# Optimization experiments

Hardware: AMD Instinct MI355X
Metric: run time of the kernel (lower is better)

## Reference

```python
import jax, jax.numpy as jnp
import numpy as np

NEG_MASK = -999999.0  # additive mask constant from the original module


def setup_inputs() -> dict:
    key = jax.random.key(0)
    k1, k2, k3, k4 = jax.random.split(key, 4)
    B, P, H, D = 64, 512, 512, 512
    premise_batch = jax.random.normal(k1, (B, P, D), dtype=jnp.float32)
    hypothesis_batch = jax.random.normal(k2, (B, H, D), dtype=jnp.float32)
    premise_mask = jax.random.randint(k3, (B, P), 0, 2, dtype=jnp.int32)
    hypothesis_mask = jax.random.randint(k4, (B, H), 0, 2, dtype=jnp.int32)
    return {
        "premise_batch": premise_batch,
        "premise_mask": premise_mask,
        "hypothesis_batch": hypothesis_batch,
        "hypothesis_mask": hypothesis_mask,
    }


def reference(premise_batch, premise_mask, hypothesis_batch, hypothesis_mask):
    # similarity: [B, P, H]
    sim = jnp.einsum("bpd,bhd->bph", premise_batch, hypothesis_batch)
    # additive -999999 masks, exactly as in the torch source
    hyp_pad = (hypothesis_mask == 0).astype(sim.dtype)[:, None, :]   # [B,1,H]
    pre_pad = (premise_mask == 0).astype(sim.dtype)[:, :, None]      # [B,P,1]
    sim_hyp = sim + NEG_MASK * hyp_pad
    sim_pre = sim + NEG_MASK * pre_pad
    attention_a = jax.nn.softmax(sim_pre, axis=2)  # softmax over hypothesis dim
    attention_b = jax.nn.softmax(sim_hyp, axis=1)  # softmax over premise dim
    attended_premises = jnp.einsum("bph,bhd->bpd", attention_a, hypothesis_batch)
    attended_hypothesis = jnp.einsum("bph,bpd->bhd", attention_b, premise_batch)
    return (attended_premises, attended_hypothesis)
```

## Files before the change

### kernel.cpp

```cpp
#include <hip/hip_runtime.h>
#include <hip/hip_bf16.h>
#include <math.h>

#define NEG_MASK -999999.0f

constexpr int BB = 64, PP = 512, HH = 512, DD = 512;

typedef _Float16 h8    __attribute__((ext_vector_type(8)));
typedef float    f32x4 __attribute__((ext_vector_type(4)));
typedef float    f32x2 __attribute__((ext_vector_type(2)));

#define MFMA16(a, b, c) __builtin_amdgcn_mfma_f32_16x16x32_f16(a, b, c, 0, 0, 0)

__device__ __forceinline__ int swz(int row, int kb) {
  return (row * 64 + kb) ^ ((row & 7) << 4);
}

__device__ __forceinline__ void gload16(const void* g, void* l) {
  __builtin_amdgcn_global_load_lds(
      (const __attribute__((address_space(1))) unsigned int*)g,
      (__attribute__((address_space(3))) unsigned int*)l, 16, 0, 0);
}

__device__ __forceinline__ void inv_swz(int x, int& row, int& kb) {
  row = ((x >> 7) << 1) | (((x >> 6) & 1) ^ ((x >> 8) & 1));
  kb = (x & 63) ^ ((row & 3) << 4);
}

__global__ __launch_bounds__(256) void tcvt(const float* __restrict__ src,
                                            _Float16* __restrict__ dst) {
  const int b = blockIdx.z;
  const int d0 = blockIdx.x * 64, n0 = blockIdx.y * 64;
  src += (size_t)b * 512 * 512;
  dst += (size_t)b * 512 * 512;
  const int dl = threadIdx.x & 63, nch = (threadIdx.x >> 6) * 16;
  const float* ps = src + (size_t)(n0 + nch) * 512 + d0 + dl;
  h8 o[2];
#pragma unroll
  for (int e = 0; e < 16; ++e)
    o[e >> 3][e & 7] = (_Float16)ps[(size_t)e * 512];
  _Float16* pd = dst + (size_t)(d0 + dl) * 512 + n0 + nch;
  *reinterpret_cast<h8*>(pd) = o[0];
  *reinterpret_cast<h8*>(pd + 8) = o[1];
}

__global__ __launch_bounds__(256, 2) void sim_mfma(const float* __restrict__ pre,
                                                   const float* __restrict__ hyp,
                                                   float* __restrict__ sim) {
  const int b = blockIdx.z;
  const int p0 = blockIdx.y * 128, h0 = blockIdx.x * 128;

  __shared__ __align__(16) char sAh[8192], sAl[8192], sBh[8192], sBl[8192];

  const int t = threadIdx.x;
  const int r = t >> 1, kh = t & 1;
  const int lane = t & 63, wid = t >> 6;
  const int l15 = lane & 15, l4 = lane >> 4;
  const int wr = (wid >> 1) * 64, wc = (wid & 1) * 64;

  f32x4 acc[4][4] = {};

  const float* pA = pre + (size_t)b * PP * DD + (size_t)(p0 + r) * DD + kh * 16;
  const float* pB = hyp + (size_t)b * HH * DD + (size_t)(h0 + r) * DD + kh * 16;

  for (int kk = 0; kk < DD; kk += 32) {
    f32x4 ra[4], rb[4];
#pragma unroll
    for (int c = 0; c < 4; ++c) {
      ra[c] = *reinterpret_cast<const f32x4*>(pA + kk + c * 4);
      rb[c] = *reinterpret_cast<const f32x4*>(pB + kk + c * 4);
    }
    __syncthreads();
    h8 vah[2], val[2], vbh[2], vbl[2];
#pragma unroll
    for (int c = 0; c < 4; ++c)
#pragma unroll
      for (int e = 0; e < 4; ++e) {
        const int idx = c * 4 + e;
        float fa = ra[c][e], fb = rb[c][e];
        _Float16 ha = (_Float16)fa, hb = (_Float16)fb;
        vah[idx >> 3][idx & 7] = ha;
        val[idx >> 3][idx & 7] = (_Float16)(fa - (float)ha);
        vbh[idx >> 3][idx & 7] = hb;
        vbl[idx >> 3][idx & 7] = (_Float16)(fb - (float)hb);
      }
    *reinterpret_cast<h8*>(sAh + swz(r, kh * 32)) = vah[0];
    *reinterpret_cast<h8*>(sAh + swz(r, kh * 32 + 16)) = vah[1];
    *reinterpret_cast<h8*>(sAl + swz(r, kh * 32)) = val[0];
    *reinterpret_cast<h8*>(sAl + swz(r, kh * 32 + 16)) = val[1];
    *reinterpret_cast<h8*>(sBh + swz(r, kh * 32)) = vbh[0];
    *reinterpret_cast<h8*>(sBh + swz(r, kh * 32 + 16)) = vbh[1];
    *reinterpret_cast<h8*>(sBl + swz(r, kh * 32)) = vbl[0];
    *reinterpret_cast<h8*>(sBl + swz(r, kh * 32 + 16)) = vbl[1];
    __syncthreads();

    h8 Ah[4], Al[4], Bh[4], Bl[4];
#pragma unroll
    for (int i = 0; i < 4; ++i) {
      Ah[i] = *reinterpret_cast<const h8*>(sAh + swz(wr + i * 16 + l15, l4 * 16));
      Al[i] = *reinterpret_cast<const h8*>(sAl + swz(wr + i * 16 + l15, l4 * 16));
      Bh[i] = *reinterpret_cast<const h8*>(sBh + swz(wc + i * 16 + l15, l4 * 16));
      Bl[i] = *reinterpret_cast<const h8*>(sBl + swz(wc + i * 16 + l15, l4 * 16));
    }
#pragma unroll
    for (int i = 0; i < 4; ++i)
#pragma unroll
      for (int j = 0; j < 4; ++j) {
        acc[i][j] = MFMA16(Ah[i], Bh[j], acc[i][j]);
        acc[i][j] = MFMA16(Ah[i], Bl[j], acc[i][j]);
        acc[i][j] = MFMA16(Al[i], Bh[j], acc[i][j]);
      }
  }

  float* S = sim + (size_t)b * PP * HH;
#pragma unroll
  for (int i = 0; i < 4; ++i)
#pragma unroll
    for (int j = 0; j < 4; ++j)
#pragma unroll
      for (int rr = 0; rr < 4; ++rr)
        S[(size_t)(p0 + wr + i * 16 + l4 * 4 + rr) * HH + h0 + wc + j * 16 + l15] =
            acc[i][j][rr];
}

__global__ __launch_bounds__(256) void stats_rows(const float* __restrict__ sim,
                                                  const int* __restrict__ pmask,
                                                  float* __restrict__ maxA,
                                                  float* __restrict__ sumA) {
  const int wid = threadIdx.x >> 6, lane = threadIdx.x & 63;
  const int row = blockIdx.x * 4 + wid;
  const float* s = sim + (size_t)row * HH + lane * 8;
  const float c = (pmask[row] == 0) ? NEG_MASK : 0.f;

  f32x4 v0 = *reinterpret_cast<const f32x4*>(s);
  f32x4 v1 = *reinterpret_cast<const f32x4*>(s + 4);
  float tv[8] = {v0[0] + c, v0[1] + c, v0[2] + c, v0[3] + c,
                 v1[0] + c, v1[1] + c, v1[2] + c, v1[3] + c};
  float m = tv[0];
#pragma unroll
  for (int e = 1; e < 8; ++e) m = fmaxf(m, tv[e]);
#pragma unroll
  for (int o = 1; o < 64; o <<= 1) m = fmaxf(m, __shfl_xor(m, o, 64));
  float sum = 0.f;
#pragma unroll
  for (int e = 0; e < 8; ++e) sum += __expf(tv[e] - m);
#pragma unroll
  for (int o = 1; o < 64; o <<= 1) sum += __shfl_xor(sum, o, 64);
  if (lane == 0) { maxA[row] = m; sumA[row] = sum; }
}

__global__ __launch_bounds__(256) void stats_cols(const float* __restrict__ sim,
                                                  const int* __restrict__ hmask,
                                                  float* __restrict__ maxB,
                                                  float* __restrict__ sumB) {
  const int b = blockIdx.y;
  const int th = threadIdx.x & 63, seg = threadIdx.x >> 6;
  const int h = blockIdx.x * 64 + th;
  const float* s = sim + (size_t)b * PP * HH + h;
  const float c = (hmask[b * HH + h] == 0) ? NEG_MASK : 0.f;

  __shared__ float red[4][64];

  float m = -3.4e38f;
  for (int p = seg * 128; p < seg * 128 + 128; ++p)
    m = fmaxf(m, s[(size_t)p * HH] + c);
  red[seg][th] = m;
  __syncthreads();
  m = fmaxf(fmaxf(red[0][th], red[1][th]), fmaxf(red[2][th], red[3][th]));

  float sum = 0.f;
  for (int p = seg * 128; p < seg * 128 + 128; ++p)
    sum += __expf((s[(size_t)p * HH] + c) - m);
  __syncthreads();
  red[seg][th] = sum;
  __syncthreads();
  if (seg == 0) {
    maxB[b * HH + h] = m;
    sumB[b * HH + h] = red[0][th] + red[1][th] + red[2][th] + red[3][th];
  }
}

__global__ __launch_bounds__(256, 3) void att_a_mfma(const float* __restrict__ sim,
                                                     const _Float16* __restrict__ hypT,
                                                     const int* __restrict__ pmask,
                                                     const float* __restrict__ maxA,
                                                     const float* __restrict__ sumA,
                                                     float* __restrict__ out) {
  const int b = blockIdx.z;
  const int p0 = blockIdx.y * 128, d0 = blockIdx.x * 128;
  const float* S = sim + (size_t)b * PP * HH;
  const _Float16* T = hypT + (size_t)b * DD * HH;

  __shared__ __align__(16) char sW[8192], sV[8192];

  const int t = threadIdx.x;
  const int lane = t & 63, wid = t >> 6;
  const int l15 = lane & 15, l4 = lane >> 4;
  const int wr = (wid >> 1) * 64, wc = (wid & 1) * 64;

  const int r = t >> 1, kh = t & 1;
  const float cA = (pmask[b * PP + p0 + r] == 0) ? NEG_MASK : 0.f;
  const float mA = maxA[b * PP + p0 + r];

  int row0, kb0, row1, kb1;
  inv_swz(t * 16, row0, kb0);
  inv_swz(4096 + t * 16, row1, kb1);
  const _Float16* srcV0 = T + (size_t)(d0 + row0) * HH + (kb0 >> 1);
  const _Float16* srcV1 = T + (size_t)(d0 + row1) * HH + (kb1 >> 1);
  void* lb0 = sV + wid * 1024;
  void* lb1 = sV + 4096 + wid * 1024;

  const float* pS = S + (size_t)(p0 + r) * HH + kh * 16;
  f32x4 rs[4];
#pragma unroll
  for (int c = 0; c < 4; ++c) rs[c] = *reinterpret_cast<const f32x4*>(pS + c * 4);

  f32x4 acc[4][4] = {};

  for (int kk = 0; kk < HH; kk += 32) {
    h8 wv[2];
#pragma unroll
    for (int c = 0; c < 4; ++c)
#pragma unroll
      for (int e = 0; e < 4; ++e) {
        const int idx = c * 4 + e;
        wv[idx >> 3][idx & 7] = (_Float16)__expf((rs[c][e] + cA) - mA);
      }
    __syncthreads();
    gload16(srcV0 + kk, lb0);
    gload16(srcV1 + kk, lb1);
    *reinterpret_cast<h8*>(sW + swz(r, kh * 32)) = wv[0];
    *reinterpret_cast<h8*>(sW + swz(r, kh * 32 + 16)) = wv[1];
    __syncthreads();
    if (kk + 32 < HH) {
#pragma unroll
      for (int c = 0; c < 4; ++c)
        rs[c] = *reinterpret_cast<const f32x4*>(pS + kk + 32 + c * 4);
    }
    h8 Wf[4], Vf[4];
#pragma unroll
    for (int i = 0; i < 4; ++i) {
      Wf[i] = *reinterpret_cast<const h8*>(sW + swz(wr + i * 16 + l15, l4 * 16));
      Vf[i] = *reinterpret_cast<const h8*>(sV + swz(wc + i * 16 + l15, l4 * 16));
    }
#pragma unroll
    for (int i = 0; i < 4; ++i)
#pragma unroll
      for (int j = 0; j < 4; ++j)
        acc[i][j] = MFMA16(Wf[i], Vf[j], acc[i][j]);
  }

  float* O = out + (size_t)b * PP * DD;
#pragma unroll
  for (int i = 0; i < 4; ++i)
#pragma unroll
    for (int rr = 0; rr < 4; ++rr) {
      const int prow = p0 + wr + i * 16 + l4 * 4 + rr;
      const float inv = 1.f / sumA[b * PP + prow];
#pragma unroll
      for (int j = 0; j < 4; ++j)
        O[(size_t)prow * DD + d0 + wc + j * 16 + l15] = acc[i][j][rr] * inv;
    }
}

__global__ __launch_bounds__(256, 3) void att_b_mfma(const float* __restrict__ sim,
                                                     const _Float16* __restrict__ preT,
                                                     const int* __restrict__ hmask,
                                                     const float* __restrict__ maxB,
                                                     const float* __restrict__ sumB,
                                                     float* __restrict__ out) {
  const int b = blockIdx.z;
  const int h0 = blockIdx.y * 128, d0 = blockIdx.x * 128;
  const float* S = sim + (size_t)b * PP * HH;
  const _Float16* T = preT + (size_t)b * DD * PP;

  __shared__ __align__(16) char sW[8192], sU[8192];

  const int t = threadIdx.x;
  const int lane = t & 63, wid = t >> 6;
  const int l15 = lane & 15, l4 = lane >> 4;
  const int wr = (wid >> 1) * 64, wc = (wid & 1) * 64;

  const int hp = t >> 2, kq = t & 3;
  float cH[2], mB[2];
#pragma unroll
  for (int hh = 0; hh < 2; ++hh) {
    const int h = h0 + hp * 2 + hh;
    cH[hh] = (hmask[b * HH + h] == 0) ? NEG_MASK : 0.f;
    mB[hh] = maxB[b * HH + h];
  }

  int row0, kb0, row1, kb1;
  inv_swz(t * 16, row0, kb0);
  inv_swz(4096 + t * 16, row1, kb1);
  const _Float16* srcU0 = T + (size_t)(d0 + row0) * PP + (kb0 >> 1);
  const _Float16* srcU1 = T + (size_t)(d0 + row1) * PP + (kb1 >> 1);
  void* lb0 = sU + wid * 1024;
  void* lb1 = sU + 4096 + wid * 1024;

  const float* pS0 = S + h0 + hp * 2;
  f32x2 rw[8];
#pragma unroll
  for (int jj = 0; jj < 8; ++jj)
    rw[jj] = *reinterpret_cast<const f32x2*>(pS0 + (size_t)(kq * 8 + jj) * HH);

  f32x4 acc[4][4] = {};

  for (int kk = 0; kk < PP; kk += 32) {
    h8 w0, w1;
#pragma unroll
    for (int jj = 0; jj < 8; ++jj) {
      w0[jj] = (_Float16)__expf((rw[jj][0] + cH[0]) - mB[0]);
      w1[jj] = (_Float16)__expf((rw[jj][1] + cH[1]) - mB[1]);
    }
    __syncthreads();
    gload16(srcU0 + kk, lb0);
    gload16(srcU1 + kk, lb1);
    *reinterpret_cast<h8*>(sW + swz(hp * 2 + 0, kq * 16)) = w0;
    *reinterpret_cast<h8*>(sW + swz(hp * 2 + 1, kq * 16)) = w1;
    __syncthreads();
    if (kk + 32 < PP) {
#pragma unroll
      for (int jj = 0; jj < 8; ++jj)
        rw[jj] = *reinterpret_cast<const f32x2*>(pS0 + (size_t)(kk + 32 + kq * 8 + jj) * HH);
    }
    h8 Wf[4], Uf[4];
#pragma unroll
    for (int i = 0; i < 4; ++i) {
      Wf[i] = *reinterpret_cast<const h8*>(sW + swz(wr + i * 16 + l15, l4 * 16));
      Uf[i] = *reinterpret_cast<const h8*>(sU + swz(wc + i * 16 + l15, l4 * 16));
    }
#pragma unroll
    for (int i = 0; i < 4; ++i)
#pragma unroll
      for (int j = 0; j < 4; ++j)
        acc[i][j] = MFMA16(Wf[i], Uf[j], acc[i][j]);
  }

  float* O = out + (size_t)b * HH * DD;
#pragma unroll
  for (int i = 0; i < 4; ++i)
#pragma unroll
    for (int rr = 0; rr < 4; ++rr) {
      const int hrow = h0 + wr + i * 16 + l4 * 4 + rr;
      const float inv = 1.f / sumB[b * HH + hrow];
#pragma unroll
      for (int j = 0; j < 4; ++j)
        O[(size_t)hrow * DD + d0 + wc + j * 16 + l15] = acc[i][j][rr] * inv;
    }
}

extern "C" void kernel_launch(void* const* d_in, const int* in_sizes, int n_in,
                              void* d_out, int out_size, void* d_ws, size_t ws_size,
                              hipStream_t stream) {
  const float* pre  = (const float*)d_in[0];
  const int* pmask  = (const int*)d_in[1];
  const float* hyp  = (const float*)d_in[2];
  const int* hmask  = (const int*)d_in[3];

  float* out0 = (float*)d_out;
  float* out1 = out0 + (size_t)BB * PP * DD;

  float* sim = (float*)d_ws;
  _Float16* hypT = (_Float16*)(sim + (size_t)BB * PP * HH);
  _Float16* preT = hypT + (size_t)BB * DD * HH;
  float* maxA = (float*)(preT + (size_t)BB * DD * PP);
  float* sumA = maxA + BB * PP;
  float* maxB = sumA + BB * PP;
  float* sumB = maxB + BB * HH;

  tcvt<<<dim3(8, 8, BB), 256, 0, stream>>>(hyp, hypT);
  tcvt<<<dim3(8, 8, BB), 256, 0, stream>>>(pre, preT);
  sim_mfma<<<dim3(HH / 128, PP / 128, BB), 256, 0, stream>>>(pre, hyp, sim);
  stats_rows<<<dim3(BB * PP / 4), 256, 0, stream>>>(sim, pmask, maxA, sumA);
  stats_cols<<<dim3(HH / 64, BB), 256, 0, stream>>>(sim, hmask, maxB, sumB);
  att_a_mfma<<<dim3(DD / 128, PP / 128, BB), 256, 0, stream>>>(sim, hypT, pmask, maxA, sumA, out0);
  att_b_mfma<<<dim3(DD / 128, HH / 128, BB), 256, 0, stream>>>(sim, preT, hmask, maxB, sumB, out1);
}
```

Before: 494.8 us.

## Transpose similarity matrix so column softmax reuses row-softmax and attention kernels

Adds a tiled LDS transpose of the similarity matrix into extra workspace. The column-wise softmax stats and the hypothesis attention then run through the same row-oriented stats and attention kernels used for the premise side. This replaces the strided column access of the old path. It also remaps block indices so neighbouring tiles of one batch land on the same XCD, and raises the occupancy hint to 4 blocks. The cost is an extra 64 MB workspace buffer and a full read/write pass over sim, with the old path kept as a fallback when the workspace is too small.

Measured after the change: 487.8 us. No clear change (-1.4%).

```diff
diff --git a/kernel.cpp b/kernel.cpp
--- a/kernel.cpp
+++ b/kernel.cpp
@@ -25,6 +25,12 @@
 __device__ __forceinline__ void inv_swz(int x, int& row, int& kb) {
   row = ((x >> 7) << 1) | (((x >> 6) & 1) ^ ((x >> 8) & 1));
   kb = (x & 63) ^ ((row & 3) << 4);
+}
+
+__device__ __forceinline__ void xcd_remap(int& bx, int& by, int& bz) {
+  int flat = blockIdx.x + 4 * blockIdx.y + 16 * blockIdx.z;
+  int nid = (flat & 7) * 128 + (flat >> 3);
+  bx = nid & 3; by = (nid >> 2) & 3; bz = nid >> 4;
 }
 
 __global__ __launch_bounds__(256) void tcvt(const float* __restrict__ src,
@@ -44,11 +50,40 @@
   *reinterpret_cast<h8*>(pd + 8) = o[1];
 }
 
-__global__ __launch_bounds__(256, 2) void sim_mfma(const float* __restrict__ pre,
+__global__ __launch_bounds__(256) void tps(const float* __restrict__ sim,
+                                           float* __restrict__ simT) {
+  const int b = blockIdx.z;
+  const int h0 = blockIdx.x * 64, p0 = blockIdx.y * 64;
+  const float* S = sim + (size_t)b * PP * HH;
+  float* T = simT + (size_t)b * HH * PP;
+
+  __shared__ float L[64 * 67];
+
+  const int tx = threadIdx.x & 15, ty = threadIdx.x >> 4;
+#pragma unroll
+  for (int pass = 0; pass < 4; ++pass) {
+    const int p = ty + pass * 16;
+    f32x4 v = *reinterpret_cast<const f32x4*>(S + (size_t)(p0 + p) * HH + h0 + tx * 4);
+#pragma unroll
+    for (int e = 0; e < 4; ++e) L[p * 67 + tx * 4 + e] = v[e];
+  }
+  __syncthreads();
+#pragma unroll
+  for (int pass = 0; pass < 4; ++pass) {
+    const int h = ty + pass * 16;
+    f32x4 w;
+#pragma unroll
+    for (int e = 0; e < 4; ++e) w[e] = L[(tx * 4 + e) * 67 + h];
+    *reinterpret_cast<f32x4*>(T + (size_t)(h0 + h) * PP + p0 + tx * 4) = w;
+  }
+}
+
+__global__ __launch_bounds__(256, 4) void sim_mfma(const float* __restrict__ pre,
                                                    const float* __restrict__ hyp,
                                                    float* __restrict__ sim) {
-  const int b = blockIdx.z;
-  const int p0 = blockIdx.y * 128, h0 = blockIdx.x * 128;
+  int bx, by, b;
+  xcd_remap(bx, by, b);
+  const int p0 = by * 128, h0 = bx * 128;
 
   __shared__ __align__(16) char sAh[8192], sAl[8192], sBh[8192], sBl[8192];
 
@@ -123,14 +158,14 @@
             acc[i][j][rr];
 }
 
-__global__ __launch_bounds__(256) void stats_rows(const float* __restrict__ sim,
-                                                  const int* __restrict__ pmask,
-                                                  float* __restrict__ maxA,
-                                                  float* __restrict__ sumA) {
+__global__ __launch_bounds__(256) void stats_rows(const float* __restrict__ S,
+                                                  const int* __restrict__ mask,
+                                                  float* __restrict__ maxO,
+                                                  float* __restrict__ sumO) {
   const int wid = threadIdx.x >> 6, lane = threadIdx.x & 63;
   const int row = blockIdx.x * 4 + wid;
-  const float* s = sim + (size_t)row * HH + lane * 8;
-  const float c = (pmask[row] == 0) ? NEG_MASK : 0.f;
+  const float* s = S + (size_t)row * 512 + lane * 8;
+  const float c = (mask[row] == 0) ? NEG_MASK : 0.f;
 
   f32x4 v0 = *reinterpret_cast<const f32x4*>(s);
   f32x4 v1 = *reinterpret_cast<const f32x4*>(s + 4);
@@ -146,7 +181,7 @@
   for (int e = 0; e < 8; ++e) sum += __expf(tv[e] - m);
 #pragma unroll
   for (int o = 1; o < 64; o <<= 1) sum += __shfl_xor(sum, o, 64);
-  if (lane == 0) { maxA[row] = m; sumA[row] = sum; }
+  if (lane == 0) { maxO[row] = m; sumO[row] = sum; }
 }
 
 __global__ __launch_bounds__(256) void stats_cols(const float* __restrict__ sim,
@@ -180,16 +215,17 @@
   }
 }
 
-__global__ __launch_bounds__(256, 3) void att_a_mfma(const float* __restrict__ sim,
-                                                     const _Float16* __restrict__ hypT,
-                                                     const int* __restrict__ pmask,
-                                                     const float* __restrict__ maxA,
-                                                     const float* __restrict__ sumA,
-                                                     float* __restrict__ out) {
-  const int b = blockIdx.z;
-  const int p0 = blockIdx.y * 128, d0 = blockIdx.x * 128;
-  const float* S = sim + (size_t)b * PP * HH;
-  const _Float16* T = hypT + (size_t)b * DD * HH;
+__global__ __launch_bounds__(256, 4) void att(const float* __restrict__ S_,
+                                              const _Float16* __restrict__ T_,
+                                              const int* __restrict__ mask,
+                                              const float* __restrict__ maxI,
+                                              const float* __restrict__ sumI,
+                                              float* __restrict__ out) {
+  int bx, by, b;
+  xcd_remap(bx, by, b);
+  const int n0 = by * 128, d0 = bx * 128;
+  const float* S = S_ + (size_t)b * 512 * 512;
+  const _Float16* T = T_ + (size_t)b * 512 * 512;
 
   __shared__ __align__(16) char sW[8192], sV[8192];
 
@@ -199,25 +235,25 @@
   const int wr = (wid >> 1) * 64, wc = (wid & 1) * 64;
 
   const int r = t >> 1, kh = t & 1;
-  const float cA = (pmask[b * PP + p0 + r] == 0) ? NEG_MASK : 0.f;
-  const float mA = maxA[b * PP + p0 + r];
+  const float cA = (mask[b * 512 + n0 + r] == 0) ? NEG_MASK : 0.f;
+  const float mA = maxI[b * 512 + n0 + r];
 
   int row0, kb0, row1, kb1;
   inv_swz(t * 16, row0, kb0);
   inv_swz(4096 + t * 16, row1, kb1);
-  const _Float16* srcV0 = T + (size_t)(d0 + row0) * HH + (kb0 >> 1);
-  const _Float16* srcV1 = T + (size_t)(d0 + row1) * HH + (kb1 >> 1);
+  const _Float16* srcV0 = T + (size_t)(d0 + row0) * 512 + (kb0 >> 1);
+  const _Float16* srcV1 = T + (size_t)(d0 + row1) * 512 + (kb1 >> 1);
   void* lb0 = sV + wid * 1024;
   void* lb1 = sV + 4096 + wid * 1024;
 
-  const float* pS = S + (size_t)(p0 + r) * HH + kh * 16;
+  const float* pS = S + (size_t)(n0 + r) * 512 + kh * 16;
   f32x4 rs[4];
 #pragma unroll
   for (int c = 0; c < 4; ++c) rs[c] = *reinterpret_cast<const f32x4*>(pS + c * 4);
 
   f32x4 acc[4][4] = {};
 
-  for (int kk = 0; kk < HH; kk += 32) {
+  for (int kk = 0; kk < 512; kk += 32) {
     h8 wv[2];
 #pragma unroll
     for (int c = 0; c < 4; ++c)
@@ -232,7 +268,7 @@
     *reinterpret_cast<h8*>(sW + swz(r, kh * 32)) = wv[0];
     *reinterpret_cast<h8*>(sW + swz(r, kh * 32 + 16)) = wv[1];
     __syncthreads();
-    if (kk + 32 < HH) {
+    if (kk + 32 < 512) {
 #pragma unroll
       for (int c = 0; c < 4; ++c)
         rs[c] = *reinterpret_cast<const f32x4*>(pS + kk + 32 + c * 4);
@@ -250,20 +286,20 @@
         acc[i][j] = MFMA16(Wf[i], Vf[j], acc[i][j]);
   }
 
-  float* O = out + (size_t)b * PP * DD;
+  float* O = out + (size_t)b * 512 * 512;
 #pragma unroll
   for (int i = 0; i < 4; ++i)
 #pragma unroll
     for (int rr = 0; rr < 4; ++rr) {
-      const int prow = p0 + wr + i * 16 + l4 * 4 + rr;
-      const float inv = 1.f / sumA[b * PP + prow];
+      const int nrow = n0 + wr + i * 16 + l4 * 4 + rr;
+      const float inv = 1.f / sumI[b * 512 + nrow];
 #pragma unroll
       for (int j = 0; j < 4; ++j)
-        O[(size_t)prow * DD + d0 + wc + j * 16 + l15] = acc[i][j][rr] * inv;
-    }
-}
-
-__global__ __launch_bounds__(256, 3) void att_b_mfma(const float* __restrict__ sim,
+        O[(size_t)nrow * 512 + d0 + wc + j * 16 + l15] = acc[i][j][rr] * inv;
+    }
+}
+
+__global__ __launch_bounds__(256, 3) void att_b_slow(const float* __restrict__ sim,
                                                      const _Float16* __restrict__ preT,
                                                      const int* __restrict__ hmask,
                                                      const float* __restrict__ maxB,
@@ -361,19 +397,30 @@
   float* out0 = (float*)d_out;
   float* out1 = out0 + (size_t)BB * PP * DD;
 
-  float* sim = (float*)d_ws;
-  _Float16* hypT = (_Float16*)(sim + (size_t)BB * PP * HH);
-  _Float16* preT = hypT + (size_t)BB * DD * HH;
-  float* maxA = (float*)(preT + (size_t)BB * DD * PP);
+  char* ws = (char*)d_ws;
+  float* sim = (float*)ws;
+  _Float16* hypT = (_Float16*)(ws + 67108864ULL);
+  _Float16* preT = (_Float16*)(ws + 100663296ULL);
+  float* maxA = (float*)(ws + 134217728ULL);
   float* sumA = maxA + BB * PP;
   float* maxB = sumA + BB * PP;
   float* sumB = maxB + BB * HH;
+  float* simT = (float*)(ws + 134742016ULL);
+  const bool big = ws_size >= 134742016ULL + 67108864ULL;
 
   tcvt<<<dim3(8, 8, BB), 256, 0, stream>>>(hyp, hypT);
   tcvt<<<dim3(8, 8, BB), 256, 0, stream>>>(pre, preT);
-  sim_mfma<<<dim3(HH / 128, PP / 128, BB), 256, 0, stream>>>(pre, hyp, sim);
+  sim_mfma<<<dim3(4, 4, BB), 256, 0, stream>>>(pre, hyp, sim);
   stats_rows<<<dim3(BB * PP / 4), 256, 0, stream>>>(sim, pmask, maxA, sumA);
-  stats_cols<<<dim3(HH / 64, BB), 256, 0, stream>>>(sim, hmask, maxB, sumB);
-  att_a_mfma<<<dim3(DD / 128, PP / 128, BB), 256, 0, stream>>>(sim, hypT, pmask, maxA, sumA, out0);
-  att_b_mfma<<<dim3(DD / 128, HH / 128, BB), 256, 0, stream>>>(sim, preT, hmask, maxB, sumB, out1);
-}
+
+  if (big) {
+    tps<<<dim3(8, 8, BB), 256, 0, stream>>>(sim, simT);
+    stats_rows<<<dim3(BB * HH / 4), 256, 0, stream>>>(simT, hmask, maxB, sumB);
+    att<<<dim3(4, 4, BB), 256, 0, stream>>>(sim, hypT, pmask, maxA, sumA, out0);
+    att<<<dim3(4, 4, BB), 256, 0, stream>>>(simT, preT, hmask, maxB, sumB, out1);
+  } else {
+    stats_cols<<<dim3(HH / 64, BB), 256, 0, stream>>>(sim, hmask, maxB, sumB);
+    att<<<dim3(4, 4, BB), 256, 0, stream>>>(sim, hypT, pmask, maxA, sumA, out0);
+    att_b_slow<<<dim3(4, 4, BB), 256, 0, stream>>>(sim, preT, hmask, maxB, sumB, out1);
+  }
+}
```
